# Performance work log

Hardware: AMD Instinct MI355X
Metric: run time of the kernel (lower is better)

Reference implementation:

```python
import jax, jax.numpy as jnp
import numpy as np

N = 50000
E = 800000
F_IN = 256
HID = 64
HEADS = 4
CLASSES = 32
NEG_SLOPE = 0.2


def setup_inputs() -> dict:
    key = jax.random.key(0)
    ks = jax.random.split(key, 10)
    x = jax.random.normal(ks[0], (N, F_IN), dtype=jnp.float32)
    edge_index = jax.random.randint(ks[1], (2, E), 0, N, dtype=jnp.int64)
    s1 = 1.0 / np.sqrt(F_IN)
    s2 = 1.0 / np.sqrt(HID * HEADS)
    W1 = jax.random.normal(ks[2], (F_IN, HEADS * HID), dtype=jnp.float32) * s1
    a_src1 = jax.random.normal(ks[3], (HEADS, HID), dtype=jnp.float32) * s1
    a_dst1 = jax.random.normal(ks[4], (HEADS, HID), dtype=jnp.float32) * s1
    b1 = jnp.zeros((HEADS * HID,), dtype=jnp.float32)
    W2 = jax.random.normal(ks[5], (HEADS * HID, CLASSES), dtype=jnp.float32) * s2
    a_src2 = jax.random.normal(ks[6], (1, CLASSES), dtype=jnp.float32) * s2
    a_dst2 = jax.random.normal(ks[7], (1, CLASSES), dtype=jnp.float32) * s2
    b2 = jnp.zeros((CLASSES,), dtype=jnp.float32)
    return {"x": x, "edge_index": edge_index, "W1": W1, "a_src1": a_src1,
            "a_dst1": a_dst1, "b1": b1, "W2": W2, "a_src2": a_src2,
            "a_dst2": a_dst2, "b2": b2}


def gat_conv(x, src, dst, W, a_src, a_dst, bias, num_nodes):
    # PyG GATConv: h = x W, per-head attention logits, segment softmax over dst,
    # scatter-weighted aggregation. src/dst already include self-loops.
    H, C = a_src.shape
    h = (x @ W).reshape(num_nodes, H, C)               # [N, H, C]
    al_s = jnp.sum(h * a_src[None], axis=-1)            # [N, H]
    al_d = jnp.sum(h * a_dst[None], axis=-1)            # [N, H]
    e = jax.nn.leaky_relu(al_s[src] + al_d[dst], NEG_SLOPE)  # [Et, H]
    m = jax.ops.segment_max(e, dst, num_segments=num_nodes)  # [N, H]
    ex = jnp.exp(e - m[dst])
    denom = jax.ops.segment_sum(ex, dst, num_segments=num_nodes)
    alpha = ex / denom[dst]                              # [Et, H]
    out = jax.ops.segment_sum(alpha[:, :, None] * h[src], dst,
                              num_segments=num_nodes)    # [N, H, C]
    return out.reshape(num_nodes, H * C) + bias


def reference(x, edge_index, W1, a_src1, a_dst1, b1, W2, a_src2, a_dst2, b2):
    num_nodes = x.shape[0]
    loop = jnp.arange(num_nodes, dtype=edge_index.dtype)
    src = jnp.concatenate([edge_index[0], loop])  # add_self_loops=True (PyG default)
    dst = jnp.concatenate([edge_index[1], loop])
    # dropout is identity in eval mode
    h = jax.nn.elu(gat_conv(x, src, dst, W1, a_src1, a_dst1, b1, num_nodes))
    out = gat_conv(h, src, dst, W2, a_src2, a_dst2, b2, num_nodes)
    return jax.nn.log_softmax(out, axis=1)
```

## Files before the change

kernel.cpp:

```cpp
#include <hip/hip_runtime.h>
#include <math.h>

#define N_NODES 50000
#define N_EDGES 800000
#define ET (N_EDGES + N_NODES)
#define NEG_SLOPE 0.2f

#define BSHIFT 8
#define NBUK ((N_NODES + 255) >> BSHIFT)
#define BCAP 4608
#define ACHUNK 4096

typedef __attribute__((ext_vector_type(8))) short s16x8;
typedef __attribute__((ext_vector_type(4))) float f32x4;
typedef __attribute__((ext_vector_type(2))) float f32x2;

__device__ __forceinline__ unsigned short f2bf(float f) {
    union { float f; unsigned u; } v; v.f = f;
    unsigned r = v.u + 0x7FFF + ((v.u >> 16) & 1);
    return (unsigned short)(r >> 16);
}
__device__ __forceinline__ float bf2f(unsigned short s) {
    union { unsigned u; float f; } v; v.u = ((unsigned)s) << 16;
    return v.f;
}
__device__ __forceinline__ uint4 pack_bf16_trunc(float4 f0, float4 f1) {
    const unsigned* a = (const unsigned*)&f0;
    const unsigned* b = (const unsigned*)&f1;
    uint4 r;
    r.x = (a[0] >> 16) | (a[1] & 0xffff0000u);
    r.y = (a[2] >> 16) | (a[3] & 0xffff0000u);
    r.z = (b[0] >> 16) | (b[1] & 0xffff0000u);
    r.w = (b[2] >> 16) | (b[3] & 0xffff0000u);
    return r;
}
__device__ __forceinline__ unsigned char f2fp8(float f) {
    return (unsigned char)(__builtin_amdgcn_cvt_pk_fp8_f32(f, f, 0, false) & 0xff);
}


__global__ __launch_bounds__(256) void k_cvtw(const float* __restrict__ W1, const float* __restrict__ W2,
                                              unsigned short* __restrict__ WT, unsigned short* __restrict__ W2T,
                                              int* __restrict__ bcur) {
    int b = blockIdx.x, k = threadIdx.x;
    if (b < 256) {
        WT[b * 256 + k] = f2bf(W1[k * 256 + b]);
    } else if (b < 288) {
        int c = b - 256;
        W2T[c * 256 + k] = f2bf(W2[k * 32 + c]);
    } else {
        if (k < NBUK) bcur[k] = 0;
    }
}


__global__ __launch_bounds__(256) void k_bin(const int* __restrict__ ei, int* __restrict__ bcur,
                                             unsigned* __restrict__ stage) {
    __shared__ unsigned sdata[ACHUNK];
    __shared__ unsigned short sv[ACHUNK];
    __shared__ int scnt[NBUK];
    __shared__ int soff[NBUK + 1];
    __shared__ int sgbase[NBUK];
    __shared__ int wssc[4];
    int tid = threadIdx.x;
    int e0 = blockIdx.x * ACHUNK;
    int nE = N_EDGES - e0;
    if (nE > ACHUNK) nE = ACHUNK;
    for (int i = tid; i < NBUK; i += 256) scnt[i] = 0;
    __syncthreads();
    for (int i = tid; i < nE; i += 256) {
        int v = ei[N_EDGES + e0 + i];
        sv[i] = (unsigned short)v;
        atomicAdd(&scnt[v >> BSHIFT], 1);
    }
    __syncthreads();
    {
        int lane = tid & 63, w = tid >> 6;
        int val = (tid < NBUK) ? scnt[tid] : 0;
        int incl = val;
        for (int o = 1; o < 64; o <<= 1) {
            int t = __shfl_up(incl, o);
            if (lane >= o) incl += t;
        }
        if (lane == 63) wssc[w] = incl;
        __syncthreads();
        int wb = 0;
        for (int i = 0; i < w; ++i) wb += wssc[i];
        if (tid < NBUK) soff[tid] = wb + incl - val;
        if (tid == 255) soff[NBUK] = wb + incl;
    }
    __syncthreads();
    if (tid < NBUK) {
        int c = scnt[tid];
        sgbase[tid] = c ? atomicAdd(&bcur[tid], c) : 0;
        scnt[tid] = soff[tid];
    }
    __syncthreads();
    for (int i = tid; i < nE; i += 256) {
        int u = ei[e0 + i];
        unsigned v = sv[i];
        int b = (int)(v >> BSHIFT);
        int pos = atomicAdd(&scnt[b], 1);
        sdata[pos] = (unsigned)u | ((v & 255u) << 16);
    }
    __syncthreads();
    for (int i = tid; i < nE; i += 256) {
        int lo = 0, hi = NBUK - 1;
        while (lo < hi) {
            int mid = (lo + hi + 1) >> 1;
            if (soff[mid] <= i) lo = mid; else hi = mid - 1;
        }
        int rel = sgbase[lo] + (i - soff[lo]);
        if (rel < BCAP) stage[(size_t)lo * BCAP + rel] = sdata[i];
    }
}


__global__ __launch_bounds__(256) void k_bukscan(const int* __restrict__ bcur, int* __restrict__ bukbase,
                                                 int* __restrict__ off) {
    __shared__ int ws[4];
    int tid = threadIdx.x, lane = tid & 63, w = tid >> 6;
    int val = 0;
    if (tid < NBUK) {
        int base = tid << BSHIFT;
        int nv = N_NODES - base;
        if (nv > 256) nv = 256;
        val = bcur[tid] + nv;
    }
    int incl = val;
    for (int o = 1; o < 64; o <<= 1) {
        int t = __shfl_up(incl, o);
        if (lane >= o) incl += t;
    }
    if (lane == 63) ws[w] = incl;
    __syncthreads();
    int wb = 0;
    for (int i = 0; i < w; ++i) wb += ws[i];
    if (tid < NBUK) bukbase[tid] = wb + incl - val;
    if (tid == 0) off[N_NODES] = ET;
}


__global__ __launch_bounds__(256) void k_build(const unsigned* __restrict__ stage,
                                               const int* __restrict__ bcur, const int* __restrict__ bukbase,
                                               int* __restrict__ off, int* __restrict__ esrc) {
    __shared__ int hist[256];
    __shared__ int lexcl[257];
    __shared__ int ws[4];
    __shared__ int outbuf[BCAP + 256];
    int b = blockIdx.x, tid = threadIdx.x;
    int n = bcur[b];
    if (n > BCAP) n = BCAP;
    int base = b << BSHIFT;
    int nv = N_NODES - base;
    if (nv > 256) nv = 256;
    hist[tid] = 0;
    __syncthreads();
    const unsigned* sg = stage + (size_t)b * BCAP;
    for (int i = tid; i < n; i += 256) atomicAdd(&hist[sg[i] >> 16], 1);
    __syncthreads();
    int lane = tid & 63, w = tid >> 6;
    int val = (tid < nv) ? hist[tid] + 1 : 0;
    int incl = val;
    for (int o = 1; o < 64; o <<= 1) {
        int t = __shfl_up(incl, o);
        if (lane >= o) incl += t;
    }
    if (lane == 63) ws[w] = incl;
    __syncthreads();
    int wb = 0;
    for (int i = 0; i < w; ++i) wb += ws[i];
    int excl = wb + incl - val;
    lexcl[tid] = excl;
    if (tid == 255) lexcl[256] = excl + val;
    int gb = bukbase[b];
    if (tid < nv) off[base + tid] = gb + excl;
    __syncthreads();
    int total = lexcl[256];
    if (tid < nv) {
        outbuf[excl] = base + tid;
        hist[tid] = 1;
    }
    __syncthreads();
    for (int i = tid; i < n; i += 256) {
        unsigned pk = sg[i];
        int vloc = (int)(pk >> 16);
        int pos = lexcl[vloc] + atomicAdd(&hist[vloc], 1);
        outbuf[pos] = (int)(pk & 0xffffu);
    }
    __syncthreads();
    for (int i = tid; i < total; i += 256) esrc[gb + i] = outbuf[i];
}


__global__ __launch_bounds__(256) void k_gemm1m(const float* __restrict__ X, const unsigned short* __restrict__ WT,
                                                const float* __restrict__ a_src, const float* __restrict__ a_dst,
                                                unsigned char* __restrict__ H8,
                                                float* __restrict__ als, float* __restrict__ ald) {
    __shared__ unsigned short As[64][40];
    __shared__ unsigned short Bs[256][40];
    int tid = threadIdx.x;
    int row0 = blockIdx.x * 64;
    int wv = tid >> 6, lane = tid & 63;
    int wm = wv & 1, wn = wv >> 1;
    int lr = lane & 15, quad = lane >> 4;
    f32x4 acc[2][8];
#pragma unroll
    for (int mt = 0; mt < 2; ++mt)
#pragma unroll
        for (int nt = 0; nt < 8; ++nt) acc[mt][nt] = (f32x4){0.f, 0.f, 0.f, 0.f};

    int ar = tid >> 2, aseg = tid & 3;
    for (int k0 = 0; k0 < 256; k0 += 32) {
        {
            int grow = row0 + ar;
            float4 f0 = make_float4(0.f, 0.f, 0.f, 0.f), f1 = f0;
            if (grow < N_NODES) {
                const float* src = X + (size_t)grow * 256 + k0 + aseg * 8;
                f0 = *(const float4*)src;
                f1 = *(const float4*)(src + 4);
            }
            *(uint4*)&As[ar][aseg * 8] = pack_bf16_trunc(f0, f1);
        }
#pragma unroll
        for (int pass = 0; pass < 4; ++pass) {
            int q = tid + pass * 256;
            int n = q >> 2, seg = q & 3;
            uint4 v = *(const uint4*)(WT + (n << 8) + k0 + seg * 8);
            *(uint4*)&Bs[n][seg * 8] = v;
        }
        __syncthreads();
        s16x8 a[2], b[8];
#pragma unroll
        for (int mt = 0; mt < 2; ++mt) a[mt] = *(const s16x8*)&As[wm * 32 + mt * 16 + lr][quad * 8];
#pragma unroll
        for (int nt = 0; nt < 8; ++nt) b[nt] = *(const s16x8*)&Bs[wn * 128 + nt * 16 + lr][quad * 8];
#pragma unroll
        for (int mt = 0; mt < 2; ++mt)
#pragma unroll
            for (int nt = 0; nt < 8; ++nt)
                acc[mt][nt] = __builtin_amdgcn_mfma_f32_16x16x32_bf16(a[mt], b[nt], acc[mt][nt], 0, 0, 0);
        __syncthreads();
    }
#pragma unroll
    for (int mt = 0; mt < 2; ++mt) {
#pragma unroll
        for (int r = 0; r < 4; ++r) {
            int row = row0 + wm * 32 + mt * 16 + quad * 4 + r;
            if (row < N_NODES) {
#pragma unroll
                for (int nt = 0; nt < 8; ++nt) {
                    int col = wn * 128 + nt * 16 + lr;
                    H8[(size_t)row * 256 + col] = f2fp8(acc[mt][nt][r]);
                }
            }
        }
    }
    float av[8], dv[8];
#pragma unroll
    for (int nt = 0; nt < 8; ++nt) {
        int col = wn * 128 + nt * 16 + lr;
        av[nt] = a_src[col];
        dv[nt] = a_dst[col];
    }
    float ps[2][8], pd[2][8];
#pragma unroll
    for (int hl = 0; hl < 2; ++hl)
#pragma unroll
        for (int i = 0; i < 8; ++i) { ps[hl][i] = 0.f; pd[hl][i] = 0.f; }
#pragma unroll
    for (int mt = 0; mt < 2; ++mt)
#pragma unroll
        for (int nt = 0; nt < 8; ++nt) {
            int hl = nt >> 2;
#pragma unroll
            for (int r = 0; r < 4; ++r) {
                float v = acc[mt][nt][r];
                ps[hl][mt * 4 + r] = fmaf(v, av[nt], ps[hl][mt * 4 + r]);
                pd[hl][mt * 4 + r] = fmaf(v, dv[nt], pd[hl][mt * 4 + r]);
            }
        }
#pragma unroll
    for (int hl = 0; hl < 2; ++hl)
#pragma unroll
        for (int i = 0; i < 8; ++i) {
            float s = ps[hl][i], d = pd[hl][i];
#pragma unroll
            for (int m = 8; m >= 1; m >>= 1) { s += __shfl_xor(s, m); d += __shfl_xor(d, m); }
            if (lr == 0) {
                int row = row0 + wm * 32 + (i >> 2) * 16 + quad * 4 + (i & 3);
                if (row < N_NODES) {
                    als[row * 4 + wn * 2 + hl] = s;
                    ald[row * 4 + wn * 2 + hl] = d;
                }
            }
        }
}


__global__ __launch_bounds__(256) void k_agg1(const unsigned* __restrict__ H8u,
                                              const float* __restrict__ als, const float* __restrict__ ald_,
                                              const int* __restrict__ off, const int* __restrict__ esrc,
                                              const float* __restrict__ b1, unsigned* __restrict__ H2p) {
    int wid = (blockIdx.x * 256 + threadIdx.x) >> 6;
    int lane = threadIdx.x & 63;
    int head = lane >> 4;
    float ald = ald_[wid * 4 + head];
    int pstart = off[wid], pend = off[wid + 1];
    float l = 0.f, ax = 0.f, ay = 0.f, az = 0.f, aw = 0.f;

    auto edge1 = [&](int u0) {
        unsigned v0 = H8u[(unsigned)u0 * 64 + lane];
        float e0 = als[(unsigned)u0 * 4 + head] + ald;
        e0 = fmaxf(e0, NEG_SLOPE * e0);
        float pw0 = __expf(e0);
        l += pw0;
        f32x2 a0 = __builtin_amdgcn_cvt_pk_f32_fp8(v0, false), b0 = __builtin_amdgcn_cvt_pk_f32_fp8(v0, true);
        ax = fmaf(pw0, a0.x, ax);
        ay = fmaf(pw0, a0.y, ay);
        az = fmaf(pw0, b0.x, az);
        aw = fmaf(pw0, b0.y, aw);
    };
    auto edge4 = [&](int4 u4) {
        unsigned v0 = H8u[(unsigned)u4.x * 64 + lane];
        unsigned v1 = H8u[(unsigned)u4.y * 64 + lane];
        unsigned v2 = H8u[(unsigned)u4.z * 64 + lane];
        unsigned v3 = H8u[(unsigned)u4.w * 64 + lane];
        float e0 = als[(unsigned)u4.x * 4 + head] + ald;
        float e1 = als[(unsigned)u4.y * 4 + head] + ald;
        float e2 = als[(unsigned)u4.z * 4 + head] + ald;
        float e3 = als[(unsigned)u4.w * 4 + head] + ald;
        e0 = fmaxf(e0, NEG_SLOPE * e0);
        e1 = fmaxf(e1, NEG_SLOPE * e1);
        e2 = fmaxf(e2, NEG_SLOPE * e2);
        e3 = fmaxf(e3, NEG_SLOPE * e3);
        float pw0 = __expf(e0), pw1 = __expf(e1), pw2 = __expf(e2), pw3 = __expf(e3);
        l += (pw0 + pw1) + (pw2 + pw3);
        f32x2 a0 = __builtin_amdgcn_cvt_pk_f32_fp8(v0, false), b0 = __builtin_amdgcn_cvt_pk_f32_fp8(v0, true);
        f32x2 a1 = __builtin_amdgcn_cvt_pk_f32_fp8(v1, false), b1v = __builtin_amdgcn_cvt_pk_f32_fp8(v1, true);
        f32x2 a2 = __builtin_amdgcn_cvt_pk_f32_fp8(v2, false), b2v = __builtin_amdgcn_cvt_pk_f32_fp8(v2, true);
        f32x2 a3 = __builtin_amdgcn_cvt_pk_f32_fp8(v3, false), b3v = __builtin_amdgcn_cvt_pk_f32_fp8(v3, true);
        ax = fmaf(pw3, a3.x, fmaf(pw2, a2.x, fmaf(pw1, a1.x, fmaf(pw0, a0.x, ax))));
        ay = fmaf(pw3, a3.y, fmaf(pw2, a2.y, fmaf(pw1, a1.y, fmaf(pw0, a0.y, ay))));
        az = fmaf(pw3, b3v.x, fmaf(pw2, b2v.x, fmaf(pw1, b1v.x, fmaf(pw0, b0.x, az))));
        aw = fmaf(pw3, b3v.y, fmaf(pw2, b2v.y, fmaf(pw1, b1v.y, fmaf(pw0, b0.y, aw))));
    };

    int p = pstart;
    int npeel = (4 - (p & 3)) & 3;
    for (int i = 0; i < npeel && p < pend; ++i, ++p) edge1(esrc[p]);
    for (; p + 7 < pend; p += 8) {
        int4 ua = *(const int4*)(esrc + p);
        int4 ub = *(const int4*)(esrc + p + 4);
        edge4(ua);
        edge4(ub);
    }
    for (; p + 3 < pend; p += 4) edge4(*(const int4*)(esrc + p));
    for (; p < pend; ++p) edge1(esrc[p]);

    float inv = 1.f / l;
    int c = lane * 4;
    float4 bb = *(const float4*)(b1 + c);
    float o0 = ax * inv + bb.x, o1 = ay * inv + bb.y, o2 = az * inv + bb.z, o3 = aw * inv + bb.w;
    o0 = o0 > 0.f ? o0 : expm1f(o0);
    o1 = o1 > 0.f ? o1 : expm1f(o1);
    o2 = o2 > 0.f ? o2 : expm1f(o2);
    o3 = o3 > 0.f ? o3 : expm1f(o3);
    unsigned pk = __builtin_amdgcn_cvt_pk_fp8_f32(o0, o1, 0, false);
    pk = __builtin_amdgcn_cvt_pk_fp8_f32(o2, o3, pk, true);
    H2p[(unsigned)wid * 64 + lane] = pk;
}


__global__ __launch_bounds__(256) void k_gemm2m(const unsigned* __restrict__ H2p,
                                                const unsigned short* __restrict__ W2T,
                                                const float* __restrict__ as2, const float* __restrict__ ad2,
                                                unsigned short* __restrict__ Gb, float* __restrict__ als2,
                                                float* __restrict__ ald2) {
    int tid = threadIdx.x;
    int wv = tid >> 6, lane = tid & 63, lr = lane & 15, quad = lane >> 4;
    int row0 = blockIdx.x * 64 + wv * 16;
    int rowA = row0 + lr;
    unsigned rA = (rowA < N_NODES) ? (unsigned)rowA : (unsigned)(N_NODES - 1);
    f32x4 acc[2];
    acc[0] = (f32x4){0.f, 0.f, 0.f, 0.f};
    acc[1] = (f32x4){0.f, 0.f, 0.f, 0.f};
#pragma unroll
    for (int k0 = 0; k0 < 256; k0 += 32) {
        uint2 d = *(const uint2*)(H2p + rA * 64 + (k0 >> 2) + quad * 2);
        f32x2 f0 = __builtin_amdgcn_cvt_pk_f32_fp8(d.x, false);
        f32x2 f1 = __builtin_amdgcn_cvt_pk_f32_fp8(d.x, true);
        f32x2 f2 = __builtin_amdgcn_cvt_pk_f32_fp8(d.y, false);
        f32x2 f3 = __builtin_amdgcn_cvt_pk_f32_fp8(d.y, true);
        union { uint4 u; s16x8 s; } cv;
        cv.u = pack_bf16_trunc(make_float4(f0.x, f0.y, f1.x, f1.y), make_float4(f2.x, f2.y, f3.x, f3.y));
        s16x8 afrag = cv.s;
        s16x8 b0 = *(const s16x8*)(W2T + lr * 256 + k0 + quad * 8);
        s16x8 b1f = *(const s16x8*)(W2T + (16 + lr) * 256 + k0 + quad * 8);
        acc[0] = __builtin_amdgcn_mfma_f32_16x16x32_bf16(afrag, b0, acc[0], 0, 0, 0);
        acc[1] = __builtin_amdgcn_mfma_f32_16x16x32_bf16(afrag, b1f, acc[1], 0, 0, 0);
    }
    float a2s = as2[lr], a2s2 = as2[16 + lr];
    float a2d = ad2[lr], a2d2 = ad2[16 + lr];
#pragma unroll
    for (int r = 0; r < 4; ++r) {
        int row = row0 + quad * 4 + r;
        float g0 = acc[0][r], g1 = acc[1][r];
        float s = g0 * a2s + g1 * a2s2;
        float dd = g0 * a2d + g1 * a2d2;
#pragma unroll
        for (int m = 8; m >= 1; m >>= 1) { s += __shfl_xor(s, m); dd += __shfl_xor(dd, m); }
        if (row < N_NODES) {
            Gb[(size_t)row * 32 + lr] = f2bf(g0);
            Gb[(size_t)row * 32 + 16 + lr] = f2bf(g1);
            if (lr == 0) { als2[row] = s; ald2[row] = dd; }
        }
    }
}


__global__ __launch_bounds__(256) void k_agg2(const unsigned short* __restrict__ Gb,
                                              const float* __restrict__ als2,
                                              const float* __restrict__ ald2_, const int* __restrict__ off,
                                              const int* __restrict__ esrc, const float* __restrict__ b2,
                                              float* __restrict__ out) {
    int gid = blockIdx.x * 256 + threadIdx.x;
    int node = gid >> 5;
    int col = gid & 31;
    if (node >= N_NODES) return;
    float ald = ald2_[node];
    int pstart = off[node], pend = off[node + 1];
    float l = 0.f, acc = 0.f;

    auto edge1 = [&](int u0) {
        float g0 = bf2f(Gb[(size_t)(unsigned)u0 * 32 + col]);
        float e0 = als2[u0] + ald;
        e0 = fmaxf(e0, NEG_SLOPE * e0);
        float pw0 = __expf(e0);
        l += pw0;
        acc = fmaf(pw0, g0, acc);
    };

    int p = pstart;
    for (; p + 7 < pend; p += 8) {
        int u0 = esrc[p], u1 = esrc[p + 1], u2 = esrc[p + 2], u3 = esrc[p + 3];
        int u4 = esrc[p + 4], u5 = esrc[p + 5], u6 = esrc[p + 6], u7 = esrc[p + 7];
        float g0 = bf2f(Gb[(size_t)(unsigned)u0 * 32 + col]);
        float g1 = bf2f(Gb[(size_t)(unsigned)u1 * 32 + col]);
        float g2 = bf2f(Gb[(size_t)(unsigned)u2 * 32 + col]);
        float g3 = bf2f(Gb[(size_t)(unsigned)u3 * 32 + col]);
        float g4 = bf2f(Gb[(size_t)(unsigned)u4 * 32 + col]);
        float g5 = bf2f(Gb[(size_t)(unsigned)u5 * 32 + col]);
        float g6 = bf2f(Gb[(size_t)(unsigned)u6 * 32 + col]);
        float g7 = bf2f(Gb[(size_t)(unsigned)u7 * 32 + col]);
        float e0 = als2[u0] + ald, e1 = als2[u1] + ald, e2 = als2[u2] + ald, e3 = als2[u3] + ald;
        float e4 = als2[u4] + ald, e5 = als2[u5] + ald, e6 = als2[u6] + ald, e7 = als2[u7] + ald;
        e0 = fmaxf(e0, NEG_SLOPE * e0); e1 = fmaxf(e1, NEG_SLOPE * e1);
        e2 = fmaxf(e2, NEG_SLOPE * e2); e3 = fmaxf(e3, NEG_SLOPE * e3);
        e4 = fmaxf(e4, NEG_SLOPE * e4); e5 = fmaxf(e5, NEG_SLOPE * e5);
        e6 = fmaxf(e6, NEG_SLOPE * e6); e7 = fmaxf(e7, NEG_SLOPE * e7);
        float pw0 = __expf(e0), pw1 = __expf(e1), pw2 = __expf(e2), pw3 = __expf(e3);
        float pw4 = __expf(e4), pw5 = __expf(e5), pw6 = __expf(e6), pw7 = __expf(e7);
        l += ((pw0 + pw1) + (pw2 + pw3)) + ((pw4 + pw5) + (pw6 + pw7));
        acc = fmaf(pw3, g3, fmaf(pw2, g2, fmaf(pw1, g1, fmaf(pw0, g0, acc))));
        acc = fmaf(pw7, g7, fmaf(pw6, g6, fmaf(pw5, g5, fmaf(pw4, g4, acc))));
    }
    for (; p < pend; ++p) edge1(esrc[p]);

    float o = acc / l + b2[col];
    float mm = o;
#pragma unroll
    for (int msk = 16; msk >= 1; msk >>= 1) mm = fmaxf(mm, __shfl_xor(mm, msk));
    float ex = __expf(o - mm);
    float s = ex;
#pragma unroll
    for (int msk = 16; msk >= 1; msk >>= 1) s += __shfl_xor(s, msk);
    out[(size_t)node * 32 + col] = o - mm - logf(s);
}


extern "C" void kernel_launch(void* const* d_in, const int* in_sizes, int n_in,
                              void* d_out, int out_size, void* d_ws, size_t ws_size,
                              hipStream_t stream) {
    const float* x   = (const float*)d_in[0];
    const int*   ei  = (const int*)d_in[1];
    const float* W1  = (const float*)d_in[2];
    const float* as1 = (const float*)d_in[3];
    const float* ad1 = (const float*)d_in[4];
    const float* b1  = (const float*)d_in[5];
    const float* W2  = (const float*)d_in[6];
    const float* as2 = (const float*)d_in[7];
    const float* ad2 = (const float*)d_in[8];
    const float* b2  = (const float*)d_in[9];
    float* out = (float*)d_out;

    char* p = (char*)d_ws;
    auto alloc = [&](size_t bytes) {
        char* r = p;
        p += (bytes + 255) & ~(size_t)255;
        return r;
    };
    unsigned char*  h8  = (unsigned char*)alloc((size_t)N_NODES * 256);
    unsigned*       h2p = (unsigned*)alloc((size_t)N_NODES * 64 * 4);
    unsigned short* wt  = (unsigned short*)alloc((size_t)256 * 256 * 2);
    unsigned short* w2t = (unsigned short*)alloc((size_t)32 * 256 * 2);
    unsigned short* g   = (unsigned short*)alloc((size_t)N_NODES * 32 * 2);
    float* als1 = (float*)alloc((size_t)N_NODES * 4 * 4);
    float* ald1 = (float*)alloc((size_t)N_NODES * 4 * 4);
    float* als2 = (float*)alloc((size_t)N_NODES * 4);
    float* ald2 = (float*)alloc((size_t)N_NODES * 4);
    int* bcur    = (int*)alloc(256 * 4);
    int* bukbase = (int*)alloc(256 * 4);
    int* off  = (int*)alloc((size_t)(N_NODES + 1) * 4);
    int* esrc = (int*)alloc((size_t)ET * 4);

    unsigned* stage = (unsigned*)h8;

    k_cvtw<<<289, 256, 0, stream>>>(W1, W2, wt, w2t, bcur);
    k_bin<<<(N_EDGES + ACHUNK - 1) / ACHUNK, 256, 0, stream>>>(ei, bcur, stage);
    k_bukscan<<<1, 256, 0, stream>>>(bcur, bukbase, off);
    k_build<<<NBUK, 256, 0, stream>>>(stage, bcur, bukbase, off, esrc);

    k_gemm1m<<<(N_NODES + 63) / 64, 256, 0, stream>>>(x, wt, as1, ad1, h8, als1, ald1);
    k_agg1<<<N_NODES / 4, 256, 0, stream>>>((const unsigned*)h8, als1, ald1, off, esrc, b1, h2p);
    k_gemm2m<<<(N_NODES + 63) / 64, 256, 0, stream>>>(h2p, w2t, as2, ad2, g, als2, ald2);
    k_agg2<<<(N_NODES + 7) / 8, 256, 0, stream>>>(g, als2, ald2, off, esrc, b2, out);
}
```

Before: 247.7 us.

## Precompute fp16 edge attention weights and store edge sources as 16-bit indices

Attention exponentials move out of the aggregation kernels into two new per-edge kernels, `k_ew1` and `k_ew2`, which write the weights as fp16. In layer 1 this removes the exp that each of the 16 lanes of a head was recomputing for every edge. Edge source indices are narrowed to 16 bits, which holds because the node count is below 65536. The aggregation loops now load 8 indices or weights per 16-byte vector load. The change adds two extra kernel launches and a write-then-read of the weight arrays, and the weights lose precision in fp16.

```diff
diff --git a/kernel.cpp b/kernel.cpp
--- a/kernel.cpp
+++ b/kernel.cpp
@@ -1,4 +1,5 @@
 #include <hip/hip_runtime.h>
+#include <hip/hip_fp16.h>
 #include <math.h>
 
 #define N_NODES 50000
@@ -23,6 +24,12 @@
 __device__ __forceinline__ float bf2f(unsigned short s) {
     union { unsigned u; float f; } v; v.u = ((unsigned)s) << 16;
     return v.f;
+}
+__device__ __forceinline__ unsigned short f2h(float f) {
+    union { _Float16 h; unsigned short s; } v; v.h = (_Float16)f; return v.s;
+}
+__device__ __forceinline__ float h2f(unsigned short s) {
+    union { unsigned short s; _Float16 h; } v; v.s = s; return (float)v.h;
 }
 __device__ __forceinline__ uint4 pack_bf16_trunc(float4 f0, float4 f1) {
     const unsigned* a = (const unsigned*)&f0;
@@ -143,7 +150,7 @@
 
 __global__ __launch_bounds__(256) void k_build(const unsigned* __restrict__ stage,
                                                const int* __restrict__ bcur, const int* __restrict__ bukbase,
-                                               int* __restrict__ off, int* __restrict__ esrc) {
+                                               int* __restrict__ off, unsigned short* __restrict__ esrc) {
     __shared__ int hist[256];
     __shared__ int lexcl[257];
     __shared__ int ws[4];
@@ -189,7 +196,7 @@
         outbuf[pos] = (int)(pk & 0xffffu);
     }
     __syncthreads();
-    for (int i = tid; i < total; i += 256) esrc[gb + i] = outbuf[i];
+    for (int i = tid; i < total; i += 256) esrc[gb + i] = (unsigned short)outbuf[i];
 }
 
 
@@ -298,22 +305,51 @@
 }
 
 
+__global__ __launch_bounds__(256) void k_ew1(const unsigned short* __restrict__ esrc, const int* __restrict__ off,
+                                             const float* __restrict__ als1, const float* __restrict__ ald1,
+                                             unsigned short* __restrict__ pw1) {
+    int v = ((blockIdx.x * 256 + threadIdx.x) >> 2);
+    if (v >= N_NODES) return;
+    int h = threadIdx.x & 3;
+    float ad = ald1[v * 4 + h];
+    int p0 = off[v], p1 = off[v + 1];
+    for (int p = p0; p < p1; ++p) {
+        int u = esrc[p];
+        float e = als1[u * 4 + h] + ad;
+        e = fmaxf(e, NEG_SLOPE * e);
+        pw1[p * 4 + h] = f2h(__expf(e));
+    }
+}
+
+
+__global__ __launch_bounds__(256) void k_ew2(const unsigned short* __restrict__ esrc, const int* __restrict__ off,
+                                             const float* __restrict__ als2, const float* __restrict__ ald2,
+                                             unsigned short* __restrict__ pw2) {
+    int v = blockIdx.x * 256 + threadIdx.x;
+    if (v >= N_NODES) return;
+    float ad = ald2[v];
+    int p0 = off[v], p1 = off[v + 1];
+    for (int p = p0; p < p1; ++p) {
+        float e = als2[esrc[p]] + ad;
+        e = fmaxf(e, NEG_SLOPE * e);
+        pw2[p] = f2h(__expf(e));
+    }
+}
+
+
 __global__ __launch_bounds__(256) void k_agg1(const unsigned* __restrict__ H8u,
-                                              const float* __restrict__ als, const float* __restrict__ ald_,
-                                              const int* __restrict__ off, const int* __restrict__ esrc,
+                                              const unsigned short* __restrict__ pw1,
+                                              const int* __restrict__ off, const unsigned short* __restrict__ esrc,
                                               const float* __restrict__ b1, unsigned* __restrict__ H2p) {
     int wid = (blockIdx.x * 256 + threadIdx.x) >> 6;
     int lane = threadIdx.x & 63;
     int head = lane >> 4;
-    float ald = ald_[wid * 4 + head];
     int pstart = off[wid], pend = off[wid + 1];
     float l = 0.f, ax = 0.f, ay = 0.f, az = 0.f, aw = 0.f;
 
-    auto edge1 = [&](int u0) {
+    auto edge1 = [&](int u0, int p) {
         unsigned v0 = H8u[(unsigned)u0 * 64 + lane];
-        float e0 = als[(unsigned)u0 * 4 + head] + ald;
-        e0 = fmaxf(e0, NEG_SLOPE * e0);
-        float pw0 = __expf(e0);
+        float pw0 = h2f(pw1[p * 4 + head]);
         l += pw0;
         f32x2 a0 = __builtin_amdgcn_cvt_pk_f32_fp8(v0, false), b0 = __builtin_amdgcn_cvt_pk_f32_fp8(v0, true);
         ax = fmaf(pw0, a0.x, ax);
@@ -321,42 +357,49 @@
         az = fmaf(pw0, b0.x, az);
         aw = fmaf(pw0, b0.y, aw);
     };
-    auto edge4 = [&](int4 u4) {
-        unsigned v0 = H8u[(unsigned)u4.x * 64 + lane];
-        unsigned v1 = H8u[(unsigned)u4.y * 64 + lane];
-        unsigned v2 = H8u[(unsigned)u4.z * 64 + lane];
-        unsigned v3 = H8u[(unsigned)u4.w * 64 + lane];
-        float e0 = als[(unsigned)u4.x * 4 + head] + ald;
-        float e1 = als[(unsigned)u4.y * 4 + head] + ald;
-        float e2 = als[(unsigned)u4.z * 4 + head] + ald;
-        float e3 = als[(unsigned)u4.w * 4 + head] + ald;
-        e0 = fmaxf(e0, NEG_SLOPE * e0);
-        e1 = fmaxf(e1, NEG_SLOPE * e1);
-        e2 = fmaxf(e2, NEG_SLOPE * e2);
-        e3 = fmaxf(e3, NEG_SLOPE * e3);
-        float pw0 = __expf(e0), pw1 = __expf(e1), pw2 = __expf(e2), pw3 = __expf(e3);
-        l += (pw0 + pw1) + (pw2 + pw3);
+
+    int p = pstart;
+    int npeel = (8 - (p & 7)) & 7;
+    for (int i = 0; i < npeel && p < pend; ++i, ++p) edge1(esrc[p], p);
+    for (; p + 7 < pend; p += 8) {
+        uint4 ue = *(const uint4*)(esrc + p);
+        unsigned u0 = ue.x & 0xffffu, u1 = ue.x >> 16, u2 = ue.y & 0xffffu, u3 = ue.y >> 16;
+        unsigned u4 = ue.z & 0xffffu, u5 = ue.z >> 16, u6 = ue.w & 0xffffu, u7 = ue.w >> 16;
+        unsigned v0 = H8u[u0 * 64 + lane];
+        unsigned v1 = H8u[u1 * 64 + lane];
+        unsigned v2 = H8u[u2 * 64 + lane];
+        unsigned v3 = H8u[u3 * 64 + lane];
+        unsigned v4 = H8u[u4 * 64 + lane];
+        unsigned v5 = H8u[u5 * 64 + lane];
+        unsigned v6 = H8u[u6 * 64 + lane];
+        unsigned v7 = H8u[u7 * 64 + lane];
+        float pw0 = h2f(pw1[(p + 0) * 4 + head]);
+        float pw1v = h2f(pw1[(p + 1) * 4 + head]);
+        float pw2v = h2f(pw1[(p + 2) * 4 + head]);
+        float pw3v = h2f(pw1[(p + 3) * 4 + head]);
+        float pw4v = h2f(pw1[(p + 4) * 4 + head]);
+        float pw5v = h2f(pw1[(p + 5) * 4 + head]);
+        float pw6v = h2f(pw1[(p + 6) * 4 + head]);
+        float pw7v = h2f(pw1[(p + 7) * 4 + head]);
+        l += ((pw0 + pw1v) + (pw2v + pw3v)) + ((pw4v + pw5v) + (pw6v + pw7v));
         f32x2 a0 = __builtin_amdgcn_cvt_pk_f32_fp8(v0, false), b0 = __builtin_amdgcn_cvt_pk_f32_fp8(v0, true);
         f32x2 a1 = __builtin_amdgcn_cvt_pk_f32_fp8(v1, false), b1v = __builtin_amdgcn_cvt_pk_f32_fp8(v1, true);
         f32x2 a2 = __builtin_amdgcn_cvt_pk_f32_fp8(v2, false), b2v = __builtin_amdgcn_cvt_pk_f32_fp8(v2, true);
         f32x2 a3 = __builtin_amdgcn_cvt_pk_f32_fp8(v3, false), b3v = __builtin_amdgcn_cvt_pk_f32_fp8(v3, true);
-        ax = fmaf(pw3, a3.x, fmaf(pw2, a2.x, fmaf(pw1, a1.x, fmaf(pw0, a0.x, ax))));
-        ay = fmaf(pw3, a3.y, fmaf(pw2, a2.y, fmaf(pw1, a1.y, fmaf(pw0, a0.y, ay))));
-        az = fmaf(pw3, b3v.x, fmaf(pw2, b2v.x, fmaf(pw1, b1v.x, fmaf(pw0, b0.x, az))));
-        aw = fmaf(pw3, b3v.y, fmaf(pw2, b2v.y, fmaf(pw1, b1v.y, fmaf(pw0, b0.y, aw))));
-    };
-
-    int p = pstart;
-    int npeel = (4 - (p & 3)) & 3;
-    for (int i = 0; i < npeel && p < pend; ++i, ++p) edge1(esrc[p]);
-    for (; p + 7 < pend; p += 8) {
-        int4 ua = *(const int4*)(esrc + p);
-        int4 ub = *(const int4*)(esrc + p + 4);
-        edge4(ua);
-        edge4(ub);
-    }
-    for (; p + 3 < pend; p += 4) edge4(*(const int4*)(esrc + p));
-    for (; p < pend; ++p) edge1(esrc[p]);
+        f32x2 a4 = __builtin_amdgcn_cvt_pk_f32_fp8(v4, false), b4v = __builtin_amdgcn_cvt_pk_f32_fp8(v4, true);
+        f32x2 a5 = __builtin_amdgcn_cvt_pk_f32_fp8(v5, false), b5v = __builtin_amdgcn_cvt_pk_f32_fp8(v5, true);
+        f32x2 a6 = __builtin_amdgcn_cvt_pk_f32_fp8(v6, false), b6v = __builtin_amdgcn_cvt_pk_f32_fp8(v6, true);
+        f32x2 a7 = __builtin_amdgcn_cvt_pk_f32_fp8(v7, false), b7v = __builtin_amdgcn_cvt_pk_f32_fp8(v7, true);
+        ax = fmaf(pw3v, a3.x, fmaf(pw2v, a2.x, fmaf(pw1v, a1.x, fmaf(pw0, a0.x, ax))));
+        ay = fmaf(pw3v, a3.y, fmaf(pw2v, a2.y, fmaf(pw1v, a1.y, fmaf(pw0, a0.y, ay))));
+        az = fmaf(pw3v, b3v.x, fmaf(pw2v, b2v.x, fmaf(pw1v, b1v.x, fmaf(pw0, b0.x, az))));
+        aw = fmaf(pw3v, b3v.y, fmaf(pw2v, b2v.y, fmaf(pw1v, b1v.y, fmaf(pw0, b0.y, aw))));
+        ax = fmaf(pw7v, a7.x, fmaf(pw6v, a6.x, fmaf(pw5v, a5.x, fmaf(pw4v, a4.x, ax))));
+        ay = fmaf(pw7v, a7.y, fmaf(pw6v, a6.y, fmaf(pw5v, a5.y, fmaf(pw4v, a4.y, ay))));
+        az = fmaf(pw7v, b7v.x, fmaf(pw6v, b6v.x, fmaf(pw5v, b5v.x, fmaf(pw4v, b4v.x, az))));
+        aw = fmaf(pw7v, b7v.y, fmaf(pw6v, b6v.y, fmaf(pw5v, b5v.y, fmaf(pw4v, b4v.y, aw))));
+    }
+    for (; p < pend; ++p) edge1(esrc[p], p);
 
     float inv = 1.f / l;
     int c = lane * 4;
@@ -420,52 +463,48 @@
 
 
 __global__ __launch_bounds__(256) void k_agg2(const unsigned short* __restrict__ Gb,
-                                              const float* __restrict__ als2,
-                                              const float* __restrict__ ald2_, const int* __restrict__ off,
-                                              const int* __restrict__ esrc, const float* __restrict__ b2,
-                                              float* __restrict__ out) {
+                                              const unsigned short* __restrict__ pw2,
+                                              const int* __restrict__ off, const unsigned short* __restrict__ esrc,
+                                              const float* __restrict__ b2, float* __restrict__ out) {
     int gid = blockIdx.x * 256 + threadIdx.x;
     int node = gid >> 5;
     int col = gid & 31;
     if (node >= N_NODES) return;
-    float ald = ald2_[node];
     int pstart = off[node], pend = off[node + 1];
     float l = 0.f, acc = 0.f;
 
-    auto edge1 = [&](int u0) {
+    auto edge1 = [&](int u0, int p) {
         float g0 = bf2f(Gb[(size_t)(unsigned)u0 * 32 + col]);
-        float e0 = als2[u0] + ald;
-        e0 = fmaxf(e0, NEG_SLOPE * e0);
-        float pw0 = __expf(e0);
+        float pw0 = h2f(pw2[p]);
         l += pw0;
         acc = fmaf(pw0, g0, acc);
     };
 
     int p = pstart;
+    int npeel = (8 - (p & 7)) & 7;
+    for (int i = 0; i < npeel && p < pend; ++i, ++p) edge1(esrc[p], p);
     for (; p + 7 < pend; p += 8) {
-        int u0 = esrc[p], u1 = esrc[p + 1], u2 = esrc[p + 2], u3 = esrc[p + 3];
-        int u4 = esrc[p + 4], u5 = esrc[p + 5], u6 = esrc[p + 6], u7 = esrc[p + 7];
-        float g0 = bf2f(Gb[(size_t)(unsigned)u0 * 32 + col]);
-        float g1 = bf2f(Gb[(size_t)(unsigned)u1 * 32 + col]);
-        float g2 = bf2f(Gb[(size_t)(unsigned)u2 * 32 + col]);
-        float g3 = bf2f(Gb[(size_t)(unsigned)u3 * 32 + col]);
-        float g4 = bf2f(Gb[(size_t)(unsigned)u4 * 32 + col]);
-        float g5 = bf2f(Gb[(size_t)(unsigned)u5 * 32 + col]);
-        float g6 = bf2f(Gb[(size_t)(unsigned)u6 * 32 + col]);
-        float g7 = bf2f(Gb[(size_t)(unsigned)u7 * 32 + col]);
-        float e0 = als2[u0] + ald, e1 = als2[u1] + ald, e2 = als2[u2] + ald, e3 = als2[u3] + ald;
-        float e4 = als2[u4] + ald, e5 = als2[u5] + ald, e6 = als2[u6] + ald, e7 = als2[u7] + ald;
-        e0 = fmaxf(e0, NEG_SLOPE * e0); e1 = fmaxf(e1, NEG_SLOPE * e1);
-        e2 = fmaxf(e2, NEG_SLOPE * e2); e3 = fmaxf(e3, NEG_SLOPE * e3);
-        e4 = fmaxf(e4, NEG_SLOPE * e4); e5 = fmaxf(e5, NEG_SLOPE * e5);
-        e6 = fmaxf(e6, NEG_SLOPE * e6); e7 = fmaxf(e7, NEG_SLOPE * e7);
-        float pw0 = __expf(e0), pw1 = __expf(e1), pw2 = __expf(e2), pw3 = __expf(e3);
-        float pw4 = __expf(e4), pw5 = __expf(e5), pw6 = __expf(e6), pw7 = __expf(e7);
-        l += ((pw0 + pw1) + (pw2 + pw3)) + ((pw4 + pw5) + (pw6 + pw7));
-        acc = fmaf(pw3, g3, fmaf(pw2, g2, fmaf(pw1, g1, fmaf(pw0, g0, acc))));
-        acc = fmaf(pw7, g7, fmaf(pw6, g6, fmaf(pw5, g5, fmaf(pw4, g4, acc))));
-    }
-    for (; p < pend; ++p) edge1(esrc[p]);
+        uint4 ue = *(const uint4*)(esrc + p);
+        unsigned u0 = ue.x & 0xffffu, u1 = ue.x >> 16, u2 = ue.y & 0xffffu, u3 = ue.y >> 16;
+        unsigned u4 = ue.z & 0xffffu, u5 = ue.z >> 16, u6 = ue.w & 0xffffu, u7 = ue.w >> 16;
+        float g0 = bf2f(Gb[(size_t)u0 * 32 + col]);
+        float g1 = bf2f(Gb[(size_t)u1 * 32 + col]);
+        float g2 = bf2f(Gb[(size_t)u2 * 32 + col]);
+        float g3 = bf2f(Gb[(size_t)u3 * 32 + col]);
+        float g4 = bf2f(Gb[(size_t)u4 * 32 + col]);
+        float g5 = bf2f(Gb[(size_t)u5 * 32 + col]);
+        float g6 = bf2f(Gb[(size_t)u6 * 32 + col]);
+        float g7 = bf2f(Gb[(size_t)u7 * 32 + col]);
+        uint4 pv = *(const uint4*)(pw2 + p);
+        float pw0 = h2f((unsigned short)(pv.x & 0xffffu)), pw1v = h2f((unsigned short)(pv.x >> 16));
+        float pw2v = h2f((unsigned short)(pv.y & 0xffffu)), pw3v = h2f((unsigned short)(pv.y >> 16));
+        float pw4v = h2f((unsigned short)(pv.z & 0xffffu)), pw5v = h2f((unsigned short)(pv.z >> 16));
+        float pw6v = h2f((unsigned short)(pv.w & 0xffffu)), pw7v = h2f((unsigned short)(pv.w >> 16));
+        l += ((pw0 + pw1v) + (pw2v + pw3v)) + ((pw4v + pw5v) + (pw6v + pw7v));
+        acc = fmaf(pw3v, g3, fmaf(pw2v, g2, fmaf(pw1v, g1, fmaf(pw0, g0, acc))));
+        acc = fmaf(pw7v, g7, fmaf(pw6v, g6, fmaf(pw5v, g5, fmaf(pw4v, g4, acc))));
+    }
+    for (; p < pend; ++p) edge1(esrc[p], p);
 
     float o = acc / l + b2[col];
     float mm = o;
@@ -504,7 +543,6 @@
     unsigned*       h2p = (unsigned*)alloc((size_t)N_NODES * 64 * 4);
     unsigned short* wt  = (unsigned short*)alloc((size_t)256 * 256 * 2);
     unsigned short* w2t = (unsigned short*)alloc((size_t)32 * 256 * 2);
-    unsigned short* g   = (unsigned short*)alloc((size_t)N_NODES * 32 * 2);
     float* als1 = (float*)alloc((size_t)N_NODES * 4 * 4);
     float* ald1 = (float*)alloc((size_t)N_NODES * 4 * 4);
     float* als2 = (float*)alloc((size_t)N_NODES * 4);
@@ -512,9 +550,12 @@
     int* bcur    = (int*)alloc(256 * 4);
     int* bukbase = (int*)alloc(256 * 4);
     int* off  = (int*)alloc((size_t)(N_NODES + 1) * 4);
-    int* esrc = (int*)alloc((size_t)ET * 4);
+    unsigned short* esrc = (unsigned short*)alloc((size_t)ET * 2);
+    unsigned short* pw1  = (unsigned short*)alloc((size_t)ET * 4 * 2);
 
     unsigned* stage = (unsigned*)h8;
+    unsigned short* g   = (unsigned short*)h8;
+    unsigned short* pw2 = (unsigned short*)(h8 + (size_t)4 * 1024 * 1024);
 
     k_cvtw<<<289, 256, 0, stream>>>(W1, W2, wt, w2t, bcur);
     k_bin<<<(N_EDGES + ACHUNK - 1) / ACHUNK, 256, 0, stream>>>(ei, bcur, stage);
@@ -522,7 +563,9 @@
     k_build<<<NBUK, 256, 0, stream>>>(stage, bcur, bukbase, off, esrc);
 
     k_gemm1m<<<(N_NODES + 63) / 64, 256, 0, stream>>>(x, wt, as1, ad1, h8, als1, ald1);
-    k_agg1<<<N_NODES / 4, 256, 0, stream>>>((const unsigned*)h8, als1, ald1, off, esrc, b1, h2p);
+    k_ew1<<<(N_NODES * 4 + 255) / 256, 256, 0, stream>>>(esrc, off, als1, ald1, pw1);
+    k_agg1<<<N_NODES / 4, 256, 0, stream>>>((const unsigned*)h8, pw1, off, esrc, b1, h2p);
     k_gemm2m<<<(N_NODES + 63) / 64, 256, 0, stream>>>(h2p, w2t, as2, ad2, g, als2, ald2);
-    k_agg2<<<(N_NODES + 7) / 8, 256, 0, stream>>>(g, als2, ald2, off, esrc, b2, out);
-}
+    k_ew2<<<(N_NODES + 255) / 256, 256, 0, stream>>>(esrc, off, als2, ald2, pw2);
+    k_agg2<<<(N_NODES * 32 + 255) / 256, 256, 0, stream>>>(g, pw2, off, esrc, b2, out);
+}
```

New measurement: 283.7 us. 14.5% more time.

## Store CSR edge sources as padded uint16 lists with pad-to-4 per node

Applied to the files above, without the earlier changes.

Edge source indices are narrowed from int32 to uint16. Each node's adjacency list is padded to a multiple of 4 with a sentinel node whose attention logit is -1e30, so it contributes zero weight. The per-node offsets are replaced by offset and count arrays, the bucket binary search in k_bin is replaced by storing the bucket id in the packed word, and workspace buffers are aliased to shrink the footprint. The aim is to halve index traffic and remove the scalar peel and tail loops in agg1, at the cost of processing some padded dummy edges and relying on node ids fitting in 16 bits.

```diff
diff --git a/kernel.cpp b/kernel.cpp
--- a/kernel.cpp
+++ b/kernel.cpp
@@ -3,13 +3,14 @@
 
 #define N_NODES 50000
 #define N_EDGES 800000
-#define ET (N_EDGES + N_NODES)
 #define NEG_SLOPE 0.2f
+#define PADU N_NODES
 
 #define BSHIFT 8
 #define NBUK ((N_NODES + 255) >> BSHIFT)
 #define BCAP 4608
 #define ACHUNK 4096
+#define ET_PAD_ALLOC 1000960
 
 typedef __attribute__((ext_vector_type(8))) short s16x8;
 typedef __attribute__((ext_vector_type(4))) float f32x4;
@@ -41,7 +42,7 @@
 
 __global__ __launch_bounds__(256) void k_cvtw(const float* __restrict__ W1, const float* __restrict__ W2,
                                               unsigned short* __restrict__ WT, unsigned short* __restrict__ W2T,
-                                              int* __restrict__ bcur) {
+                                              int* __restrict__ bcur, float* __restrict__ als1) {
     int b = blockIdx.x, k = threadIdx.x;
     if (b < 256) {
         WT[b * 256 + k] = f2bf(W1[k * 256 + b]);
@@ -50,6 +51,7 @@
         W2T[c * 256 + k] = f2bf(W2[k * 32 + c]);
     } else {
         if (k < NBUK) bcur[k] = 0;
+        if (k >= 196 && k < 200) als1[N_NODES * 4 + (k - 196)] = -1e30f;
     }
 }
 
@@ -101,23 +103,19 @@
         unsigned v = sv[i];
         int b = (int)(v >> BSHIFT);
         int pos = atomicAdd(&scnt[b], 1);
-        sdata[pos] = (unsigned)u | ((v & 255u) << 16);
+        sdata[pos] = (unsigned)u | ((v & 255u) << 16) | ((unsigned)b << 24);
     }
     __syncthreads();
     for (int i = tid; i < nE; i += 256) {
-        int lo = 0, hi = NBUK - 1;
-        while (lo < hi) {
-            int mid = (lo + hi + 1) >> 1;
-            if (soff[mid] <= i) lo = mid; else hi = mid - 1;
-        }
-        int rel = sgbase[lo] + (i - soff[lo]);
-        if (rel < BCAP) stage[(size_t)lo * BCAP + rel] = sdata[i];
-    }
-}
-
-
-__global__ __launch_bounds__(256) void k_bukscan(const int* __restrict__ bcur, int* __restrict__ bukbase,
-                                                 int* __restrict__ off) {
+        unsigned pk = sdata[i];
+        int buk = (int)(pk >> 24);
+        int rel = sgbase[buk] + (i - soff[buk]);
+        if (rel < BCAP) stage[(size_t)buk * BCAP + rel] = pk;
+    }
+}
+
+
+__global__ __launch_bounds__(256) void k_bukscan(const int* __restrict__ bcur, int* __restrict__ bukbase) {
     __shared__ int ws[4];
     int tid = threadIdx.x, lane = tid & 63, w = tid >> 6;
     int val = 0;
@@ -125,7 +123,7 @@
         int base = tid << BSHIFT;
         int nv = N_NODES - base;
         if (nv > 256) nv = 256;
-        val = bcur[tid] + nv;
+        val = (bcur[tid] + 4 * nv + 3) & ~3;
     }
     int incl = val;
     for (int o = 1; o < 64; o <<= 1) {
@@ -137,17 +135,17 @@
     int wb = 0;
     for (int i = 0; i < w; ++i) wb += ws[i];
     if (tid < NBUK) bukbase[tid] = wb + incl - val;
-    if (tid == 0) off[N_NODES] = ET;
 }
 
 
 __global__ __launch_bounds__(256) void k_build(const unsigned* __restrict__ stage,
                                                const int* __restrict__ bcur, const int* __restrict__ bukbase,
-                                               int* __restrict__ off, int* __restrict__ esrc) {
+                                               int* __restrict__ offp, int* __restrict__ ecnt,
+                                               unsigned short* __restrict__ esrc) {
     __shared__ int hist[256];
     __shared__ int lexcl[257];
     __shared__ int ws[4];
-    __shared__ int outbuf[BCAP + 256];
+    __shared__ int outbuf[5632];
     int b = blockIdx.x, tid = threadIdx.x;
     int n = bcur[b];
     if (n > BCAP) n = BCAP;
@@ -157,11 +155,12 @@
     hist[tid] = 0;
     __syncthreads();
     const unsigned* sg = stage + (size_t)b * BCAP;
-    for (int i = tid; i < n; i += 256) atomicAdd(&hist[sg[i] >> 16], 1);
+    for (int i = tid; i < n; i += 256) atomicAdd(&hist[(sg[i] >> 16) & 0xFF], 1);
     __syncthreads();
     int lane = tid & 63, w = tid >> 6;
-    int val = (tid < nv) ? hist[tid] + 1 : 0;
-    int incl = val;
+    int c = (tid < nv) ? hist[tid] + 1 : 0;
+    int r = (tid < nv) ? ((c + 3) & ~3) : 0;
+    int incl = r;
     for (int o = 1; o < 64; o <<= 1) {
         int t = __shfl_up(incl, o);
         if (lane >= o) incl += t;
@@ -170,26 +169,30 @@
     __syncthreads();
     int wb = 0;
     for (int i = 0; i < w; ++i) wb += ws[i];
-    int excl = wb + incl - val;
+    int excl = wb + incl - r;
     lexcl[tid] = excl;
-    if (tid == 255) lexcl[256] = excl + val;
+    if (tid == 255) lexcl[256] = excl + r;
     int gb = bukbase[b];
-    if (tid < nv) off[base + tid] = gb + excl;
+    if (tid < nv) {
+        offp[base + tid] = gb + excl;
+        ecnt[base + tid] = c;
+    }
     __syncthreads();
     int total = lexcl[256];
     if (tid < nv) {
         outbuf[excl] = base + tid;
+        for (int j = excl + c; j < excl + r; ++j) outbuf[j] = PADU;
         hist[tid] = 1;
     }
     __syncthreads();
     for (int i = tid; i < n; i += 256) {
         unsigned pk = sg[i];
-        int vloc = (int)(pk >> 16);
+        int vloc = (int)((pk >> 16) & 0xFF);
         int pos = lexcl[vloc] + atomicAdd(&hist[vloc], 1);
         outbuf[pos] = (int)(pk & 0xffffu);
     }
     __syncthreads();
-    for (int i = tid; i < total; i += 256) esrc[gb + i] = outbuf[i];
+    for (int i = tid; i < total; i += 256) esrc[gb + i] = (unsigned short)outbuf[i];
 }
 
 
@@ -300,36 +303,28 @@
 
 __global__ __launch_bounds__(256) void k_agg1(const unsigned* __restrict__ H8u,
                                               const float* __restrict__ als, const float* __restrict__ ald_,
-                                              const int* __restrict__ off, const int* __restrict__ esrc,
+                                              const int* __restrict__ offp, const int* __restrict__ ecnt,
+                                              const unsigned short* __restrict__ esrc,
                                               const float* __restrict__ b1, unsigned* __restrict__ H2p) {
     int wid = (blockIdx.x * 256 + threadIdx.x) >> 6;
     int lane = threadIdx.x & 63;
     int head = lane >> 4;
     float ald = ald_[wid * 4 + head];
-    int pstart = off[wid], pend = off[wid + 1];
+    int pstart = offp[wid];
+    int rend = pstart + ((ecnt[wid] + 3) & ~3);
     float l = 0.f, ax = 0.f, ay = 0.f, az = 0.f, aw = 0.f;
 
-    auto edge1 = [&](int u0) {
-        unsigned v0 = H8u[(unsigned)u0 * 64 + lane];
-        float e0 = als[(unsigned)u0 * 4 + head] + ald;
-        e0 = fmaxf(e0, NEG_SLOPE * e0);
-        float pw0 = __expf(e0);
-        l += pw0;
-        f32x2 a0 = __builtin_amdgcn_cvt_pk_f32_fp8(v0, false), b0 = __builtin_amdgcn_cvt_pk_f32_fp8(v0, true);
-        ax = fmaf(pw0, a0.x, ax);
-        ay = fmaf(pw0, a0.y, ay);
-        az = fmaf(pw0, b0.x, az);
-        aw = fmaf(pw0, b0.y, aw);
-    };
-    auto edge4 = [&](int4 u4) {
-        unsigned v0 = H8u[(unsigned)u4.x * 64 + lane];
-        unsigned v1 = H8u[(unsigned)u4.y * 64 + lane];
-        unsigned v2 = H8u[(unsigned)u4.z * 64 + lane];
-        unsigned v3 = H8u[(unsigned)u4.w * 64 + lane];
-        float e0 = als[(unsigned)u4.x * 4 + head] + ald;
-        float e1 = als[(unsigned)u4.y * 4 + head] + ald;
-        float e2 = als[(unsigned)u4.z * 4 + head] + ald;
-        float e3 = als[(unsigned)u4.w * 4 + head] + ald;
+    auto quad = [&](unsigned ua, unsigned ub) {
+        int u0 = (int)(ua & 0xffffu), u1 = (int)(ua >> 16);
+        int u2 = (int)(ub & 0xffffu), u3 = (int)(ub >> 16);
+        unsigned v0 = H8u[(unsigned)min(u0, N_NODES - 1) * 64 + lane];
+        unsigned v1 = H8u[(unsigned)min(u1, N_NODES - 1) * 64 + lane];
+        unsigned v2 = H8u[(unsigned)min(u2, N_NODES - 1) * 64 + lane];
+        unsigned v3 = H8u[(unsigned)min(u3, N_NODES - 1) * 64 + lane];
+        float e0 = als[u0 * 4 + head] + ald;
+        float e1 = als[u1 * 4 + head] + ald;
+        float e2 = als[u2 * 4 + head] + ald;
+        float e3 = als[u3 * 4 + head] + ald;
         e0 = fmaxf(e0, NEG_SLOPE * e0);
         e1 = fmaxf(e1, NEG_SLOPE * e1);
         e2 = fmaxf(e2, NEG_SLOPE * e2);
@@ -347,16 +342,16 @@
     };
 
     int p = pstart;
-    int npeel = (4 - (p & 3)) & 3;
-    for (int i = 0; i < npeel && p < pend; ++i, ++p) edge1(esrc[p]);
-    for (; p + 7 < pend; p += 8) {
-        int4 ua = *(const int4*)(esrc + p);
-        int4 ub = *(const int4*)(esrc + p + 4);
-        edge4(ua);
-        edge4(ub);
-    }
-    for (; p + 3 < pend; p += 4) edge4(*(const int4*)(esrc + p));
-    for (; p < pend; ++p) edge1(esrc[p]);
+    for (; p + 7 < rend; p += 8) {
+        uint2 ua = *(const uint2*)(esrc + p);
+        uint2 ub = *(const uint2*)(esrc + p + 4);
+        quad(ua.x, ua.y);
+        quad(ub.x, ub.y);
+    }
+    if (p < rend) {
+        uint2 ua = *(const uint2*)(esrc + p);
+        quad(ua.x, ua.y);
+    }
 
     float inv = 1.f / l;
     int c = lane * 4;
@@ -421,15 +416,17 @@
 
 __global__ __launch_bounds__(256) void k_agg2(const unsigned short* __restrict__ Gb,
                                               const float* __restrict__ als2,
-                                              const float* __restrict__ ald2_, const int* __restrict__ off,
-                                              const int* __restrict__ esrc, const float* __restrict__ b2,
+                                              const float* __restrict__ ald2_, const int* __restrict__ offp,
+                                              const int* __restrict__ ecnt,
+                                              const unsigned short* __restrict__ esrc, const float* __restrict__ b2,
                                               float* __restrict__ out) {
     int gid = blockIdx.x * 256 + threadIdx.x;
     int node = gid >> 5;
     int col = gid & 31;
     if (node >= N_NODES) return;
     float ald = ald2_[node];
-    int pstart = off[node], pend = off[node + 1];
+    int pstart = offp[node];
+    int pend = pstart + ecnt[node];
     float l = 0.f, acc = 0.f;
 
     auto edge1 = [&](int u0) {
@@ -440,30 +437,31 @@
         l += pw0;
         acc = fmaf(pw0, g0, acc);
     };
-
-    int p = pstart;
-    for (; p + 7 < pend; p += 8) {
-        int u0 = esrc[p], u1 = esrc[p + 1], u2 = esrc[p + 2], u3 = esrc[p + 3];
-        int u4 = esrc[p + 4], u5 = esrc[p + 5], u6 = esrc[p + 6], u7 = esrc[p + 7];
+    auto quad = [&](unsigned ua, unsigned ub) {
+        int u0 = (int)(ua & 0xffffu), u1 = (int)(ua >> 16);
+        int u2 = (int)(ub & 0xffffu), u3 = (int)(ub >> 16);
         float g0 = bf2f(Gb[(size_t)(unsigned)u0 * 32 + col]);
         float g1 = bf2f(Gb[(size_t)(unsigned)u1 * 32 + col]);
         float g2 = bf2f(Gb[(size_t)(unsigned)u2 * 32 + col]);
         float g3 = bf2f(Gb[(size_t)(unsigned)u3 * 32 + col]);
-        float g4 = bf2f(Gb[(size_t)(unsigned)u4 * 32 + col]);
-        float g5 = bf2f(Gb[(size_t)(unsigned)u5 * 32 + col]);
-        float g6 = bf2f(Gb[(size_t)(unsigned)u6 * 32 + col]);
-        float g7 = bf2f(Gb[(size_t)(unsigned)u7 * 32 + col]);
         float e0 = als2[u0] + ald, e1 = als2[u1] + ald, e2 = als2[u2] + ald, e3 = als2[u3] + ald;
-        float e4 = als2[u4] + ald, e5 = als2[u5] + ald, e6 = als2[u6] + ald, e7 = als2[u7] + ald;
         e0 = fmaxf(e0, NEG_SLOPE * e0); e1 = fmaxf(e1, NEG_SLOPE * e1);
         e2 = fmaxf(e2, NEG_SLOPE * e2); e3 = fmaxf(e3, NEG_SLOPE * e3);
-        e4 = fmaxf(e4, NEG_SLOPE * e4); e5 = fmaxf(e5, NEG_SLOPE * e5);
-        e6 = fmaxf(e6, NEG_SLOPE * e6); e7 = fmaxf(e7, NEG_SLOPE * e7);
         float pw0 = __expf(e0), pw1 = __expf(e1), pw2 = __expf(e2), pw3 = __expf(e3);
-        float pw4 = __expf(e4), pw5 = __expf(e5), pw6 = __expf(e6), pw7 = __expf(e7);
-        l += ((pw0 + pw1) + (pw2 + pw3)) + ((pw4 + pw5) + (pw6 + pw7));
+        l += (pw0 + pw1) + (pw2 + pw3);
         acc = fmaf(pw3, g3, fmaf(pw2, g2, fmaf(pw1, g1, fmaf(pw0, g0, acc))));
-        acc = fmaf(pw7, g7, fmaf(pw6, g6, fmaf(pw5, g5, fmaf(pw4, g4, acc))));
+    };
+
+    int p = pstart;
+    for (; p + 7 < pend; p += 8) {
+        uint2 ua = *(const uint2*)(esrc + p);
+        uint2 ub = *(const uint2*)(esrc + p + 4);
+        quad(ua.x, ua.y);
+        quad(ub.x, ub.y);
+    }
+    for (; p + 3 < pend; p += 4) {
+        uint2 ua = *(const uint2*)(esrc + p);
+        quad(ua.x, ua.y);
     }
     for (; p < pend; ++p) edge1(esrc[p]);
 
@@ -501,28 +499,30 @@
         return r;
     };
     unsigned char*  h8  = (unsigned char*)alloc((size_t)N_NODES * 256);
-    unsigned*       h2p = (unsigned*)alloc((size_t)N_NODES * 64 * 4);
+    unsigned char*  h2pr= (unsigned char*)alloc((size_t)N_NODES * 64 * 4);
     unsigned short* wt  = (unsigned short*)alloc((size_t)256 * 256 * 2);
     unsigned short* w2t = (unsigned short*)alloc((size_t)32 * 256 * 2);
-    unsigned short* g   = (unsigned short*)alloc((size_t)N_NODES * 32 * 2);
-    float* als1 = (float*)alloc((size_t)N_NODES * 4 * 4);
+    float* als1 = (float*)alloc(((size_t)N_NODES * 4 + 4) * 4);
     float* ald1 = (float*)alloc((size_t)N_NODES * 4 * 4);
     float* als2 = (float*)alloc((size_t)N_NODES * 4);
     float* ald2 = (float*)alloc((size_t)N_NODES * 4);
     int* bcur    = (int*)alloc(256 * 4);
     int* bukbase = (int*)alloc(256 * 4);
-    int* off  = (int*)alloc((size_t)(N_NODES + 1) * 4);
-    int* esrc = (int*)alloc((size_t)ET * 4);
-
-    unsigned* stage = (unsigned*)h8;
-
-    k_cvtw<<<289, 256, 0, stream>>>(W1, W2, wt, w2t, bcur);
+    int* offp = (int*)alloc((size_t)N_NODES * 4);
+    int* ecnt = (int*)alloc((size_t)N_NODES * 4);
+    unsigned short* esrc = (unsigned short*)alloc((size_t)ET_PAD_ALLOC * 2);
+
+    unsigned* stage = (unsigned*)h2pr;
+    unsigned* h2p = (unsigned*)h2pr;
+    unsigned short* g = (unsigned short*)h8;
+
+    k_cvtw<<<289, 256, 0, stream>>>(W1, W2, wt, w2t, bcur, als1);
     k_bin<<<(N_EDGES + ACHUNK - 1) / ACHUNK, 256, 0, stream>>>(ei, bcur, stage);
-    k_bukscan<<<1, 256, 0, stream>>>(bcur, bukbase, off);
-    k_build<<<NBUK, 256, 0, stream>>>(stage, bcur, bukbase, off, esrc);
+    k_bukscan<<<1, 256, 0, stream>>>(bcur, bukbase);
+    k_build<<<NBUK, 256, 0, stream>>>(stage, bcur, bukbase, offp, ecnt, esrc);
 
     k_gemm1m<<<(N_NODES + 63) / 64, 256, 0, stream>>>(x, wt, as1, ad1, h8, als1, ald1);
-    k_agg1<<<N_NODES / 4, 256, 0, stream>>>((const unsigned*)h8, als1, ald1, off, esrc, b1, h2p);
+    k_agg1<<<N_NODES / 4, 256, 0, stream>>>((const unsigned*)h8, als1, ald1, offp, ecnt, esrc, b1, h2p);
     k_gemm2m<<<(N_NODES + 63) / 64, 256, 0, stream>>>(h2p, w2t, as2, ad2, g, als2, ald2);
-    k_agg2<<<(N_NODES + 7) / 8, 256, 0, stream>>>(g, als2, ald2, off, esrc, b2, out);
-}
+    k_agg2<<<(N_NODES * 32 + 255) / 256, 256, 0, stream>>>(g, als2, ald2, offp, ecnt, esrc, b2, out);
+}
```

Measured after the change: 227.1 us. -8.3%, faster.
